# Kernel tuning notes

Measured on AMD Instinct MI355X. Metric: run time of the kernel, lower is better.

The kernel has to match this reference:

```python
import jax, jax.numpy as jnp
import numpy as np

NEG = -1000000000.0

def setup_inputs() -> dict:
    key = jax.random.key(0)
    k1, k2, k3, k4 = jax.random.split(key, 4)
    B, S, D = 8, 4096, 256
    query = jax.random.normal(k1, (B, S, D), dtype=jnp.float32)
    k_ = jax.random.normal(k2, (B, S, D), dtype=jnp.float32)
    value = jax.random.normal(k3, (B, S, D), dtype=jnp.float32)
    mask = jax.random.bernoulli(k4, 0.1, (B, S, 1))  # True = masked
    return {"query": query, "key": k_, "value": value, "mask": mask}

def reference(query, key, value, mask):
    # a: [B,S,1] sum of squares of query; b: [B,S,1] for key
    a = jnp.sum(query * query, axis=-1, keepdims=True)
    b = jnp.sum(key * key, axis=-1, keepdims=True)
    # s1 = (K^T / b) @ V  -> [B, D, D]; divide each key row s by b_s
    s1 = jnp.einsum('bsd,bse->bde', key / b, value)
    # score = Q / a, masked rows set to -1e9
    score = query / a
    score = jnp.where(mask, NEG, score)
    s2 = jnp.einsum('bsd,bde->bse', score, s1)
    return s2 / query.shape[-1]
```

## Files before the change

### kernel.cpp

```cpp
#include <hip/hip_runtime.h>

#define BB 8
#define SS 4096
#define DD 256
#define NEGV -1000000000.0f
#define NCH (SS / 32)

typedef float f32x4 __attribute__((ext_vector_type(4)));
typedef short s16x8 __attribute__((ext_vector_type(8)));

static __device__ __forceinline__ unsigned short f2bf(float x) {
  unsigned int u = __builtin_bit_cast(unsigned int, x);
  u += 0x7fffu + ((u >> 16) & 1u);
  return (unsigned short)(u >> 16);
}

static __device__ __forceinline__ void gload_lds16(
    const unsigned short* __restrict__ g, unsigned short* l) {
  __builtin_amdgcn_global_load_lds(
      (const __attribute__((address_space(1))) void*)g,
      (__attribute__((address_space(3))) void*)l, 16, 0, 0);
}

__global__ __launch_bounds__(256, 4) void prep_kernel(
    const float* __restrict__ Q, const float* __restrict__ K,
    const float* __restrict__ V, const int* __restrict__ mask,
    unsigned short* __restrict__ QS, unsigned short* __restrict__ KT,
    unsigned short* __restrict__ VT) {
  __shared__ unsigned short tile[32 * 260];
  const int b = blockIdx.y;
  const int sc = blockIdx.x;
  const int s0 = sc * 32;
  const int tid = threadIdx.x;
  const int w = tid >> 6, l = tid & 63;

  if (blockIdx.z == 0) {
    float4 reg[8];
    float ps[8];
    int mk[8];
#pragma unroll
    for (int it = 0; it < 8; ++it) {
      const int row = it * 4 + w;
      reg[it] = *(const float4*)(Q + ((size_t)b * SS + s0 + row) * DD + l * 4);
    }
#pragma unroll
    for (int it = 0; it < 8; ++it) mk[it] = mask[b * SS + s0 + it * 4 + w];
    __builtin_amdgcn_sched_barrier(0);
#pragma unroll
    for (int it = 0; it < 8; ++it)
      ps[it] = reg[it].x * reg[it].x + reg[it].y * reg[it].y +
               reg[it].z * reg[it].z + reg[it].w * reg[it].w;
#pragma unroll
    for (int off = 32; off; off >>= 1)
#pragma unroll
      for (int it = 0; it < 8; ++it) ps[it] += __shfl_xor(ps[it], off);
#pragma unroll
    for (int it = 0; it < 8; ++it) {
      const int row = it * 4 + w;
      const float ca = mk[it] ? 0.0f : (1.0f / ps[it]);
      const float aa = mk[it] ? NEGV : 0.0f;
      ushort4 o;
      o.x = f2bf(reg[it].x * ca + aa);
      o.y = f2bf(reg[it].y * ca + aa);
      o.z = f2bf(reg[it].z * ca + aa);
      o.w = f2bf(reg[it].w * ca + aa);
      *(ushort4*)(QS + ((size_t)b * SS + s0 + row) * DD + l * 4) = o;
    }
    return;
  }

  const int isK = (blockIdx.z == 1);
  const float* __restrict__ src = isK ? K : V;
  unsigned short* __restrict__ dst = isK ? KT : VT;

  float4 reg[8];
  float ps[8];
#pragma unroll
  for (int it = 0; it < 8; ++it) {
    const int row = it * 4 + w;
    reg[it] = *(const float4*)(src + ((size_t)b * SS + s0 + row) * DD + l * 4);
  }
  __builtin_amdgcn_sched_barrier(0);
#pragma unroll
  for (int it = 0; it < 8; ++it)
    ps[it] = reg[it].x * reg[it].x + reg[it].y * reg[it].y +
             reg[it].z * reg[it].z + reg[it].w * reg[it].w;
  float scl[8];
  if (isK) {
#pragma unroll
    for (int off = 32; off; off >>= 1)
#pragma unroll
      for (int it = 0; it < 8; ++it) ps[it] += __shfl_xor(ps[it], off);
#pragma unroll
    for (int it = 0; it < 8; ++it) scl[it] = 1.0f / ps[it];
  } else {
#pragma unroll
    for (int it = 0; it < 8; ++it) scl[it] = 1.0f;
  }
#pragma unroll
  for (int it = 0; it < 8; ++it) {
    const int row = it * 4 + w;
    ushort4 o;
    o.x = f2bf(reg[it].x * scl[it]);
    o.y = f2bf(reg[it].y * scl[it]);
    o.z = f2bf(reg[it].z * scl[it]);
    o.w = f2bf(reg[it].w * scl[it]);
    *(ushort4*)(tile + row * 260 + l * 4) = o;
  }
  __syncthreads();
  const size_t gbase = ((size_t)(b * NCH + sc) * DD + tid) * 32;
#pragma unroll
  for (int c = 0; c < 4; ++c) {
    union { unsigned short h[8]; uint4 v; } u;
#pragma unroll
    for (int j = 0; j < 8; ++j) u.h[j] = tile[(c * 8 + j) * 260 + tid];
    *(uint4*)(dst + gbase + c * 8) = u.v;
  }
}

__global__ __launch_bounds__(256) void p2_kernel(
    const unsigned short* __restrict__ KT, const unsigned short* __restrict__ VT,
    float* __restrict__ part, int iters) {
  __shared__ unsigned short vt_l[2][2][128 * 32];
  __shared__ unsigned short kt_l[2][2][128 * 32];
  const int b = blockIdx.z;
  const int d0 = (blockIdx.x & 1) * 128;
  const int e0 = (blockIdx.x >> 1) * 128;
  const int tid = threadIdx.x;
  const int w = tid >> 6, l = tid & 63;
  const int wr = w & 1, wc = w >> 1;
  const int quad = l >> 4, mr = l & 15;

  f32x4 acc[4][4];
#pragma unroll
  for (int i = 0; i < 4; ++i)
#pragma unroll
    for (int j = 0; j < 4; ++j) acc[i][j] = (f32x4){0.f, 0.f, 0.f, 0.f};

  auto stage = [&](int buf, int ks) {
    const int c0 = (blockIdx.y * iters + ks) * 2;
#pragma unroll
    for (int h = 0; h < 2; ++h) {
      const size_t vch = ((size_t)(b * NCH + c0 + h) * DD + e0) * 32 + l * 8;
      const size_t kch = ((size_t)(b * NCH + c0 + h) * DD + d0) * 32 + l * 8;
#pragma unroll
      for (int g = 0; g < 2; ++g) {
        const int r0 = w * 32 + g * 16;
        gload_lds16(VT + vch + (size_t)r0 * 32, &vt_l[buf][h][r0 * 32]);
        gload_lds16(KT + kch + (size_t)r0 * 32, &kt_l[buf][h][r0 * 32]);
      }
    }
  };

  stage(0, 0);
  __syncthreads();
  int cur = 0;
  for (int ks = 0; ks < iters; ++ks) {
    if (ks + 1 < iters) stage(cur ^ 1, ks + 1);
#pragma unroll
    for (int kh = 0; kh < 2; ++kh) {
      s16x8 af[4], bfr[4];
#pragma unroll
      for (int i = 0; i < 4; ++i)
        af[i] = *(const s16x8*)(&vt_l[cur][kh][(wr * 64 + i * 16 + mr) * 32 + quad * 8]);
#pragma unroll
      for (int j = 0; j < 4; ++j)
        bfr[j] = *(const s16x8*)(&kt_l[cur][kh][(wc * 64 + j * 16 + mr) * 32 + quad * 8]);
#pragma unroll
      for (int i = 0; i < 4; ++i)
#pragma unroll
        for (int j = 0; j < 4; ++j)
          acc[i][j] = __builtin_amdgcn_mfma_f32_16x16x32_bf16(af[i], bfr[j],
                                                              acc[i][j], 0, 0, 0);
    }
    __syncthreads();
    cur ^= 1;
  }

  float* pb = part + ((size_t)blockIdx.y * BB + b) * DD * DD;
#pragma unroll
  for (int i = 0; i < 4; ++i) {
    const int e = e0 + wr * 64 + i * 16 + quad * 4;
#pragma unroll
    for (int j = 0; j < 4; ++j) {
      const int d = d0 + wc * 64 + j * 16 + mr;
      float* p = pb + (size_t)e * DD + d;
#pragma unroll
      for (int r = 0; r < 4; ++r) p[(size_t)r * DD] = acc[i][j][r];
    }
  }
}

__global__ __launch_bounds__(256) void reduce_kernel(
    const float* __restrict__ part, unsigned short* __restrict__ s1b,
    int split) {
  const size_t i4 = ((size_t)blockIdx.x * 256 + threadIdx.x) * 4;
  float ax = 0.f, ay = 0.f, az = 0.f, aw = 0.f;
  for (int p = 0; p < split; ++p) {
    const float4 v = *(const float4*)(part + (size_t)p * (BB * DD * DD) + i4);
    ax += v.x; ay += v.y; az += v.z; aw += v.w;
  }
  ushort4 o;
  o.x = f2bf(ax); o.y = f2bf(ay); o.z = f2bf(az); o.w = f2bf(aw);
  *(ushort4*)(s1b + i4) = o;
}

__global__ __launch_bounds__(256) void p3_kernel(
    const unsigned short* __restrict__ QS, const unsigned short* __restrict__ s1b,
    float* __restrict__ out) {
  __shared__ unsigned short qs_l[2][2][128 * 32];
  __shared__ unsigned short s1_l[2][2][128 * 32];
  const int b = blockIdx.z;
  const int e0 = blockIdx.x * 128;
  const int s0 = blockIdx.y * 128;
  const int tid = threadIdx.x;
  const int w = tid >> 6, l = tid & 63;
  const int wr = w & 1, wc = w >> 1;
  const int quad = l >> 4, mr = l & 15;
  const int lr = l >> 2;
  const int lc = (l & 3) * 8;

  f32x4 acc[4][4];
#pragma unroll
  for (int i = 0; i < 4; ++i)
#pragma unroll
    for (int j = 0; j < 4; ++j) acc[i][j] = (f32x4){0.f, 0.f, 0.f, 0.f};

  auto stage = [&](int buf, int ks) {
    const int dc = ks * 64;
#pragma unroll
    for (int h = 0; h < 2; ++h)
#pragma unroll
      for (int g = 0; g < 2; ++g) {
        const int r0 = w * 32 + g * 16;
        gload_lds16(QS + ((size_t)b * SS + s0 + r0 + lr) * DD + dc + h * 32 + lc,
                    &qs_l[buf][h][r0 * 32]);
        gload_lds16(s1b + ((size_t)b * DD + e0 + r0 + lr) * DD + dc + h * 32 + lc,
                    &s1_l[buf][h][r0 * 32]);
      }
  };

  stage(0, 0);
  __syncthreads();
  int cur = 0;
  for (int ks = 0; ks < 4; ++ks) {
    if (ks + 1 < 4) stage(cur ^ 1, ks + 1);
#pragma unroll
    for (int kh = 0; kh < 2; ++kh) {
      s16x8 af[4], bfr[4];
#pragma unroll
      for (int i = 0; i < 4; ++i)
        af[i] = *(const s16x8*)(&qs_l[cur][kh][(wr * 64 + i * 16 + mr) * 32 + quad * 8]);
#pragma unroll
      for (int j = 0; j < 4; ++j)
        bfr[j] = *(const s16x8*)(&s1_l[cur][kh][(wc * 64 + j * 16 + mr) * 32 + quad * 8]);
#pragma unroll
      for (int i = 0; i < 4; ++i)
#pragma unroll
        for (int j = 0; j < 4; ++j)
          acc[i][j] = __builtin_amdgcn_mfma_f32_16x16x32_bf16(af[i], bfr[j],
                                                              acc[i][j], 0, 0, 0);
    }
    __syncthreads();
    cur ^= 1;
  }

#pragma unroll
  for (int i = 0; i < 4; ++i) {
    const int s = s0 + wr * 64 + i * 16 + quad * 4;
#pragma unroll
    for (int j = 0; j < 4; ++j) {
      const int e = e0 + wc * 64 + j * 16 + mr;
      float* p = out + ((size_t)b * SS + s) * DD + e;
#pragma unroll
      for (int r = 0; r < 4; ++r) p[(size_t)r * DD] = acc[i][j][r] * (1.0f / DD);
    }
  }
}

extern "C" void kernel_launch(void* const* d_in, const int* in_sizes, int n_in,
                              void* d_out, int out_size, void* d_ws,
                              size_t ws_size, hipStream_t stream) {
  const float* Q = (const float*)d_in[0];
  const float* K = (const float*)d_in[1];
  const float* V = (const float*)d_in[2];
  const int* mask = (const int*)d_in[3];
  float* out = (float*)d_out;

  char* ws = (char*)d_ws;
  const size_t MB = (size_t)1024 * 1024;
  unsigned short* QS = (unsigned short*)(ws);
  unsigned short* KT = (unsigned short*)(ws + 16 * MB);
  unsigned short* VT = (unsigned short*)(ws + 32 * MB);
  float* part = (float*)(ws + 48 * MB);

  const int split = (ws_size >= (size_t)82 * MB) ? 16 : 8;
  const int iters = SS / (64 * split);
  unsigned short* s1b =
      (unsigned short*)(ws + 48 * MB + (size_t)split * 2 * MB);

  prep_kernel<<<dim3(SS / 32, BB, 3), 256, 0, stream>>>(Q, K, V, mask, QS, KT,
                                                        VT);
  p2_kernel<<<dim3(4, split, BB), 256, 0, stream>>>(KT, VT, part, iters);
  reduce_kernel<<<dim3(512), 256, 0, stream>>>(part, s1b, split);
  p3_kernel<<<dim3(2, SS / 128, BB), 256, 0, stream>>>(QS, s1b, out);
}
```

Before: 174.3 us.

## Stage prep inputs through LDS via async global-to-LDS loads with swizzle

The prep kernel now loads each 32-row fp32 tile straight into shared memory with global_load_lds, using an XOR swizzle so reads are free of bank conflicts. Each row is then handled by 8 threads, which cuts the norm reduction to three shuffles instead of six per row and lets the Q output go out as 16-byte stores. This is meant to reduce shuffle work and make loads and stores wider. In exchange it uses more LDS per block (occupancy hint lowered from 4 to 3) and adds a barrier before any compute.

```diff
diff --git a/kernel.cpp b/kernel.cpp
--- a/kernel.cpp
+++ b/kernel.cpp
@@ -21,100 +21,87 @@
       (const __attribute__((address_space(1))) void*)g,
       (__attribute__((address_space(3))) void*)l, 16, 0, 0);
 }
-
-__global__ __launch_bounds__(256, 4) void prep_kernel(
+static __device__ __forceinline__ void gload_lds16f(
+    const float* __restrict__ g, float* l) {
+  __builtin_amdgcn_global_load_lds(
+      (const __attribute__((address_space(1))) void*)g,
+      (__attribute__((address_space(3))) void*)l, 16, 0, 0);
+}
+
+__global__ __launch_bounds__(256, 3) void prep_kernel(
     const float* __restrict__ Q, const float* __restrict__ K,
     const float* __restrict__ V, const int* __restrict__ mask,
     unsigned short* __restrict__ QS, unsigned short* __restrict__ KT,
     unsigned short* __restrict__ VT) {
-  __shared__ unsigned short tile[32 * 260];
+  __shared__ float tf[32 * 256];
+  __shared__ unsigned short t2[32 * 264];
   const int b = blockIdx.y;
   const int sc = blockIdx.x;
   const int s0 = sc * 32;
   const int tid = threadIdx.x;
   const int w = tid >> 6, l = tid & 63;
-
-  if (blockIdx.z == 0) {
-    float4 reg[8];
-    float ps[8];
-    int mk[8];
-#pragma unroll
-    for (int it = 0; it < 8; ++it) {
-      const int row = it * 4 + w;
-      reg[it] = *(const float4*)(Q + ((size_t)b * SS + s0 + row) * DD + l * 4);
-    }
-#pragma unroll
-    for (int it = 0; it < 8; ++it) mk[it] = mask[b * SS + s0 + it * 4 + w];
-    __builtin_amdgcn_sched_barrier(0);
-#pragma unroll
-    for (int it = 0; it < 8; ++it)
-      ps[it] = reg[it].x * reg[it].x + reg[it].y * reg[it].y +
-               reg[it].z * reg[it].z + reg[it].w * reg[it].w;
-#pragma unroll
-    for (int off = 32; off; off >>= 1)
-#pragma unroll
-      for (int it = 0; it < 8; ++it) ps[it] += __shfl_xor(ps[it], off);
-#pragma unroll
-    for (int it = 0; it < 8; ++it) {
-      const int row = it * 4 + w;
-      const float ca = mk[it] ? 0.0f : (1.0f / ps[it]);
-      const float aa = mk[it] ? NEGV : 0.0f;
-      ushort4 o;
-      o.x = f2bf(reg[it].x * ca + aa);
-      o.y = f2bf(reg[it].y * ca + aa);
-      o.z = f2bf(reg[it].z * ca + aa);
-      o.w = f2bf(reg[it].w * ca + aa);
-      *(ushort4*)(QS + ((size_t)b * SS + s0 + row) * DD + l * 4) = o;
+  const int z = blockIdx.z;
+  const float* __restrict__ src = (z == 0) ? Q : ((z == 1) ? K : V);
+
+#pragma unroll
+  for (int g = 0; g < 8; ++g) {
+    const int row = w * 8 + g;
+    gload_lds16f(src + ((size_t)b * SS + s0 + row) * DD + 4 * (l ^ g),
+                 &tf[row * 256]);
+  }
+  __syncthreads();
+
+  const int row = tid >> 3, g8 = tid & 7, r7 = row & 7;
+  f32x4 v[8];
+#pragma unroll
+  for (int j = 0; j < 8; ++j)
+    v[j] = *(const f32x4*)&tf[row * 256 + g8 * 32 + 4 * (j ^ r7)];
+  float ps = 0.f;
+#pragma unroll
+  for (int j = 0; j < 8; ++j)
+    ps += v[j].x * v[j].x + v[j].y * v[j].y + v[j].z * v[j].z + v[j].w * v[j].w;
+  ps += __shfl_xor(ps, 1);
+  ps += __shfl_xor(ps, 2);
+  ps += __shfl_xor(ps, 4);
+
+  if (z == 0) {
+    const int mk = mask[b * SS + s0 + row];
+    const float ca = mk ? 0.0f : (1.0f / ps);
+    const float aa = mk ? NEGV : 0.0f;
+    unsigned short* qrow = QS + ((size_t)b * SS + s0 + row) * DD + g8 * 32;
+#pragma unroll
+    for (int c = 0; c < 4; ++c) {
+      const f32x4 a0 = v[2 * c], a1 = v[2 * c + 1];
+      union { unsigned short h[8]; uint4 u; } o;
+      o.h[0] = f2bf(a0.x * ca + aa); o.h[1] = f2bf(a0.y * ca + aa);
+      o.h[2] = f2bf(a0.z * ca + aa); o.h[3] = f2bf(a0.w * ca + aa);
+      o.h[4] = f2bf(a1.x * ca + aa); o.h[5] = f2bf(a1.y * ca + aa);
+      o.h[6] = f2bf(a1.z * ca + aa); o.h[7] = f2bf(a1.w * ca + aa);
+      *(uint4*)(qrow + c * 8) = o.u;
     }
     return;
   }
 
-  const int isK = (blockIdx.z == 1);
-  const float* __restrict__ src = isK ? K : V;
-  unsigned short* __restrict__ dst = isK ? KT : VT;
-
-  float4 reg[8];
-  float ps[8];
-#pragma unroll
-  for (int it = 0; it < 8; ++it) {
-    const int row = it * 4 + w;
-    reg[it] = *(const float4*)(src + ((size_t)b * SS + s0 + row) * DD + l * 4);
-  }
-  __builtin_amdgcn_sched_barrier(0);
-#pragma unroll
-  for (int it = 0; it < 8; ++it)
-    ps[it] = reg[it].x * reg[it].x + reg[it].y * reg[it].y +
-             reg[it].z * reg[it].z + reg[it].w * reg[it].w;
-  float scl[8];
-  if (isK) {
-#pragma unroll
-    for (int off = 32; off; off >>= 1)
-#pragma unroll
-      for (int it = 0; it < 8; ++it) ps[it] += __shfl_xor(ps[it], off);
-#pragma unroll
-    for (int it = 0; it < 8; ++it) scl[it] = 1.0f / ps[it];
-  } else {
-#pragma unroll
-    for (int it = 0; it < 8; ++it) scl[it] = 1.0f;
-  }
-#pragma unroll
-  for (int it = 0; it < 8; ++it) {
-    const int row = it * 4 + w;
-    ushort4 o;
-    o.x = f2bf(reg[it].x * scl[it]);
-    o.y = f2bf(reg[it].y * scl[it]);
-    o.z = f2bf(reg[it].z * scl[it]);
-    o.w = f2bf(reg[it].w * scl[it]);
-    *(ushort4*)(tile + row * 260 + l * 4) = o;
-  }
-  __syncthreads();
+  const float scl = (z == 1) ? (1.0f / ps) : 1.0f;
+#pragma unroll
+  for (int c = 0; c < 4; ++c) {
+    const f32x4 a0 = v[2 * c], a1 = v[2 * c + 1];
+    union { unsigned short h[8]; uint4 u; } o;
+    o.h[0] = f2bf(a0.x * scl); o.h[1] = f2bf(a0.y * scl);
+    o.h[2] = f2bf(a0.z * scl); o.h[3] = f2bf(a0.w * scl);
+    o.h[4] = f2bf(a1.x * scl); o.h[5] = f2bf(a1.y * scl);
+    o.h[6] = f2bf(a1.z * scl); o.h[7] = f2bf(a1.w * scl);
+    *(uint4*)&t2[row * 264 + g8 * 32 + c * 8] = o.u;
+  }
+  __syncthreads();
+  unsigned short* __restrict__ dst = (z == 1) ? KT : VT;
   const size_t gbase = ((size_t)(b * NCH + sc) * DD + tid) * 32;
 #pragma unroll
   for (int c = 0; c < 4; ++c) {
-    union { unsigned short h[8]; uint4 v; } u;
-#pragma unroll
-    for (int j = 0; j < 8; ++j) u.h[j] = tile[(c * 8 + j) * 260 + tid];
-    *(uint4*)(dst + gbase + c * 8) = u.v;
+    union { unsigned short h[8]; uint4 u; } u;
+#pragma unroll
+    for (int j = 0; j < 8; ++j) u.h[j] = t2[(c * 8 + j) * 264 + tid];
+    *(uint4*)(dst + gbase + c * 8) = u.u;
   }
 }
 
```

Result: no change. 176.2 us (+1.0%).

## Replace split-K partial buffers and reduction with atomic accumulation

Applied to the files above, without the earlier changes.

p2_kernel now accumulates its split-K partial products straight into one fp32 S1 buffer with atomicAdd, instead of writing 16 separate partial slabs that a reduce kernel then sums. A fourth z-slice in prep_kernel zeroes that buffer, and a small kernel converts it to bf16. This removes writing and reading about 32MB of partials, at the cost of atomic contention and non-deterministic summation order. The sched_barrier hints in prep are also dropped.

```diff
diff --git a/kernel.cpp b/kernel.cpp
--- a/kernel.cpp
+++ b/kernel.cpp
@@ -5,6 +5,7 @@
 #define DD 256
 #define NEGV -1000000000.0f
 #define NCH (SS / 32)
+#define SPLIT 16
 
 typedef float f32x4 __attribute__((ext_vector_type(4)));
 typedef short s16x8 __attribute__((ext_vector_type(8)));
@@ -26,15 +27,22 @@
     const float* __restrict__ Q, const float* __restrict__ K,
     const float* __restrict__ V, const int* __restrict__ mask,
     unsigned short* __restrict__ QS, unsigned short* __restrict__ KT,
-    unsigned short* __restrict__ VT) {
+    unsigned short* __restrict__ VT, float* __restrict__ s1f) {
   __shared__ unsigned short tile[32 * 260];
   const int b = blockIdx.y;
   const int sc = blockIdx.x;
   const int s0 = sc * 32;
   const int tid = threadIdx.x;
   const int w = tid >> 6, l = tid & 63;
-
-  if (blockIdx.z == 0) {
+  const int z = blockIdx.z;
+
+  if (z == 3) {
+    const size_t i = ((size_t)(blockIdx.y * (SS / 32) + blockIdx.x) * 256 + tid) * 2;
+    *(float2*)(s1f + i) = (float2){0.f, 0.f};
+    return;
+  }
+
+  if (z == 0) {
     float4 reg[8];
     float ps[8];
     int mk[8];
@@ -45,7 +53,6 @@
     }
 #pragma unroll
     for (int it = 0; it < 8; ++it) mk[it] = mask[b * SS + s0 + it * 4 + w];
-    __builtin_amdgcn_sched_barrier(0);
 #pragma unroll
     for (int it = 0; it < 8; ++it)
       ps[it] = reg[it].x * reg[it].x + reg[it].y * reg[it].y +
@@ -69,7 +76,7 @@
     return;
   }
 
-  const int isK = (blockIdx.z == 1);
+  const int isK = (z == 1);
   const float* __restrict__ src = isK ? K : V;
   unsigned short* __restrict__ dst = isK ? KT : VT;
 
@@ -80,7 +87,6 @@
     const int row = it * 4 + w;
     reg[it] = *(const float4*)(src + ((size_t)b * SS + s0 + row) * DD + l * 4);
   }
-  __builtin_amdgcn_sched_barrier(0);
 #pragma unroll
   for (int it = 0; it < 8; ++it)
     ps[it] = reg[it].x * reg[it].x + reg[it].y * reg[it].y +
@@ -120,7 +126,7 @@
 
 __global__ __launch_bounds__(256) void p2_kernel(
     const unsigned short* __restrict__ KT, const unsigned short* __restrict__ VT,
-    float* __restrict__ part, int iters) {
+    float* __restrict__ s1f, int iters) {
   __shared__ unsigned short vt_l[2][2][128 * 32];
   __shared__ unsigned short kt_l[2][2][128 * 32];
   const int b = blockIdx.z;
@@ -177,7 +183,7 @@
     cur ^= 1;
   }
 
-  float* pb = part + ((size_t)blockIdx.y * BB + b) * DD * DD;
+  float* pb = s1f + (size_t)b * DD * DD;
 #pragma unroll
   for (int i = 0; i < 4; ++i) {
     const int e = e0 + wr * 64 + i * 16 + quad * 4;
@@ -186,23 +192,20 @@
       const int d = d0 + wc * 64 + j * 16 + mr;
       float* p = pb + (size_t)e * DD + d;
 #pragma unroll
-      for (int r = 0; r < 4; ++r) p[(size_t)r * DD] = acc[i][j][r];
-    }
-  }
-}
-
-__global__ __launch_bounds__(256) void reduce_kernel(
-    const float* __restrict__ part, unsigned short* __restrict__ s1b,
-    int split) {
-  const size_t i4 = ((size_t)blockIdx.x * 256 + threadIdx.x) * 4;
-  float ax = 0.f, ay = 0.f, az = 0.f, aw = 0.f;
-  for (int p = 0; p < split; ++p) {
-    const float4 v = *(const float4*)(part + (size_t)p * (BB * DD * DD) + i4);
-    ax += v.x; ay += v.y; az += v.z; aw += v.w;
-  }
-  ushort4 o;
-  o.x = f2bf(ax); o.y = f2bf(ay); o.z = f2bf(az); o.w = f2bf(aw);
-  *(ushort4*)(s1b + i4) = o;
+      for (int r = 0; r < 4; ++r) atomicAdd(p + (size_t)r * DD, acc[i][j][r]);
+    }
+  }
+}
+
+__global__ __launch_bounds__(256) void cvt_kernel(
+    const float* __restrict__ s1f, unsigned short* __restrict__ s1b) {
+  const size_t i8 = ((size_t)blockIdx.x * 256 + threadIdx.x) * 8;
+  const float4 v0 = *(const float4*)(s1f + i8);
+  const float4 v1 = *(const float4*)(s1f + i8 + 4);
+  union { unsigned short h[8]; uint4 v; } o;
+  o.h[0] = f2bf(v0.x); o.h[1] = f2bf(v0.y); o.h[2] = f2bf(v0.z); o.h[3] = f2bf(v0.w);
+  o.h[4] = f2bf(v1.x); o.h[5] = f2bf(v1.y); o.h[6] = f2bf(v1.z); o.h[7] = f2bf(v1.w);
+  *(uint4*)(s1b + i8) = o.v;
 }
 
 __global__ __launch_bounds__(256) void p3_kernel(
@@ -292,16 +295,14 @@
   unsigned short* QS = (unsigned short*)(ws);
   unsigned short* KT = (unsigned short*)(ws + 16 * MB);
   unsigned short* VT = (unsigned short*)(ws + 32 * MB);
-  float* part = (float*)(ws + 48 * MB);
-
-  const int split = (ws_size >= (size_t)82 * MB) ? 16 : 8;
-  const int iters = SS / (64 * split);
-  unsigned short* s1b =
-      (unsigned short*)(ws + 48 * MB + (size_t)split * 2 * MB);
-
-  prep_kernel<<<dim3(SS / 32, BB, 3), 256, 0, stream>>>(Q, K, V, mask, QS, KT,
-                                                        VT);
-  p2_kernel<<<dim3(4, split, BB), 256, 0, stream>>>(KT, VT, part, iters);
-  reduce_kernel<<<dim3(512), 256, 0, stream>>>(part, s1b, split);
+  float* s1f = (float*)(ws + 48 * MB);
+  unsigned short* s1b = (unsigned short*)(ws + 50 * MB);
+
+  const int iters = SS / (64 * SPLIT);
+
+  prep_kernel<<<dim3(SS / 32, BB, 4), 256, 0, stream>>>(Q, K, V, mask, QS, KT,
+                                                        VT, s1f);
+  p2_kernel<<<dim3(4, SPLIT, BB), 256, 0, stream>>>(KT, VT, s1f, iters);
+  cvt_kernel<<<dim3(BB * DD * DD / (8 * 256)), 256, 0, stream>>>(s1f, s1b);
   p3_kernel<<<dim3(2, SS / 128, BB), 256, 0, stream>>>(QS, s1b, out);
 }
```

After: 187.1 us. 7.3% more time.
